# Kernel optimization log

Hardware: AMD Instinct MI355X
Metric: run time of the kernel (lower is better)

The kernel has to match this reference:

```python
import jax, jax.numpy as jnp
import numpy as np

B, C, T, V, Ks = 32, 64, 64, 325, 2

def setup_inputs() -> dict:
    key = jax.random.key(0)
    k1, k2, k3, k4 = jax.random.split(key, 4)
    x = jax.random.normal(k1, (B, C, T, V), dtype=jnp.float32)
    gso = jax.random.normal(k2, (V, V), dtype=jnp.float32)
    weight = jax.random.normal(k3, (Ks, C, C), dtype=jnp.float32) * (1.0 / np.sqrt(C))
    bias = jax.random.normal(k4, (C,), dtype=jnp.float32) * 0.05
    return {"x": x, "gso": gso, "weight": weight, "bias": bias}

def reference(x, gso, weight, bias):
    # Align: c_in == c_out -> identity
    xp = jnp.transpose(x, (0, 2, 3, 1))            # [B, T, V, C]
    x1 = jnp.einsum('hi,btij->bthj', gso, xp)      # Chebyshev T1 = L @ x
    xs = jnp.stack([xp, x1], axis=2)               # [B, T, Ks, V, C]
    gc = jnp.einsum('btkhi,kij->bthj', xs, weight) + bias  # [B, T, V, C]
    out = jnp.transpose(gc, (0, 3, 1, 2)) + x      # residual, [B, C, T, V]
    return out
```

## Files before the change

### kernel.cpp

```cpp
#include <hip/hip_runtime.h>


typedef __bf16 bf16x8 __attribute__((ext_vector_type(8)));
typedef float f32x4 __attribute__((ext_vector_type(4)));

#define XROW 360
#define QROW 136
#define NFRAG 512

__device__ __forceinline__ float bf2f(unsigned short u) {
  union { unsigned int i; float f; } t;
  t.i = ((unsigned int)u) << 16;
  return t.f;
}
__device__ __forceinline__ unsigned short f2bf_hw(float f) {
  __bf16 b = (__bf16)f;
  union { __bf16 b; unsigned short u; } t;
  t.b = b;
  return t.u;
}

__global__ void prep_kernel(const float* __restrict__ gso,
                            const float* __restrict__ weight,
                            unsigned short* __restrict__ gfrag,
                            unsigned short* __restrict__ wt) {
  int idx = blockIdx.x * 256 + threadIdx.x;
  if (idx < 22 * 11 * NFRAG) {
    int fid = idx >> 9, r = idx & 511;
    int l = r >> 3, j = r & 7;
    int mt = fid / 11, s = fid - 11 * mt;
    int v = (mt << 4) + (l & 15);
    int u = (s << 5) + ((l >> 4) << 3) + j;
    unsigned short val = 0;
    if (v < 325 && u < 325) val = f2bf_hw(gso[v * 325 + u]);
    gfrag[idx] = val;
  }
  if (idx < 2 * 64 * 64) {
    int k = idx >> 12, r = idx & 4095, c = r >> 6, i = r & 63;
    wt[idx] = f2bf_hw(weight[(k << 12) | (i << 6) | c]);
  }
}

__global__ __launch_bounds__(1024, 4) void gconv_kernel(
    const float* __restrict__ x,
    const float* __restrict__ bias,
    const unsigned short* __restrict__ gfrag,
    const unsigned short* __restrict__ wt,
    float* __restrict__ out) {
  __shared__ unsigned short Xr[64 * XROW];
  __shared__ unsigned short XY[352 * QROW];

  const int bid = blockIdx.x;
  const int b = bid >> 6, t = bid & 63;
  const int tid = threadIdx.x;
  const int xbase = b * 1331200 + t * 325;

  {
    const int c1 = tid >> 4;
    const int u0 = tid & 15;
    const float* xrow = &x[xbase + c1 * 20800];
    unsigned short* xr = &Xr[c1 * XROW];
    unsigned short* xyc = &XY[c1];
#pragma unroll 11
    for (int k = 0; k < 22; ++k) {
      const int u = u0 + 16 * k;
      float val = (u < 325) ? xrow[u] : 0.f;
      unsigned short us = f2bf_hw(val);
      xr[u] = us;
      xyc[u * QROW] = us;
    }
  }
  __syncthreads();

  const int wid = tid >> 6, lane = tid & 63;
  const int quad = lane >> 4, l16 = lane & 15;
  const int koff = quad * 8;

  {
    const int cn = (wid & 1) * 32;
    bf16x8 bX0[11], bX1[11];
#pragma unroll
    for (int s = 0; s < 11; ++s) {
      bX0[s] = *reinterpret_cast<const bf16x8*>(&Xr[(cn + l16) * XROW + s * 32 + koff]);
      bX1[s] = *reinterpret_cast<const bf16x8*>(&Xr[(cn + 16 + l16) * XROW + s * 32 + koff]);
    }
    for (int mt = (wid >> 1); mt < 22; mt += 8) {
      const unsigned short* gp = &gfrag[(mt * 11) * NFRAG + lane * 8];
      f32x4 acc0 = {0.f, 0.f, 0.f, 0.f};
      f32x4 acc1 = {0.f, 0.f, 0.f, 0.f};
#pragma unroll
      for (int s = 0; s < 11; ++s) {
        bf16x8 ag = *reinterpret_cast<const bf16x8*>(gp + s * NFRAG);
        acc0 = __builtin_amdgcn_mfma_f32_16x16x32_bf16(ag, bX0[s], acc0, 0, 0, 0);
        acc1 = __builtin_amdgcn_mfma_f32_16x16x32_bf16(ag, bX1[s], acc1, 0, 0, 0);
      }
      const int vr = mt * 16 + quad * 4;
#pragma unroll
      for (int r = 0; r < 4; ++r) {
        XY[(vr + r) * QROW + 64 + cn + l16] = f2bf_hw(acc0[r]);
        XY[(vr + r) * QROW + 64 + cn + 16 + l16] = f2bf_hw(acc1[r]);
      }
    }
  }
  __syncthreads();

  {
    const int cb = (wid & 3) * 16;
    bf16x8 aW[4];
#pragma unroll
    for (int s = 0; s < 4; ++s)
      aW[s] = *reinterpret_cast<const bf16x8*>(
          &wt[((s >> 1) * 64 + cb + l16) * 64 + (s & 1) * 32 + koff]);
    float bias_f[4];
#pragma unroll
    for (int r = 0; r < 4; ++r) bias_f[r] = bias[cb + quad * 4 + r];

    for (int n = (wid >> 2); n < 22; n += 4) {
      const int vb = n * 16;
      const unsigned short* xyp = &XY[(vb + l16) * QROW];
      bf16x8 bx0 = *reinterpret_cast<const bf16x8*>(xyp + koff);
      bf16x8 bx1 = *reinterpret_cast<const bf16x8*>(xyp + 32 + koff);
      bf16x8 by0 = *reinterpret_cast<const bf16x8*>(xyp + 64 + koff);
      bf16x8 by1 = *reinterpret_cast<const bf16x8*>(xyp + 96 + koff);
      f32x4 acc = {0.f, 0.f, 0.f, 0.f};
      acc = __builtin_amdgcn_mfma_f32_16x16x32_bf16(aW[0], bx0, acc, 0, 0, 0);
      acc = __builtin_amdgcn_mfma_f32_16x16x32_bf16(aW[1], bx1, acc, 0, 0, 0);
      acc = __builtin_amdgcn_mfma_f32_16x16x32_bf16(aW[2], by0, acc, 0, 0, 0);
      acc = __builtin_amdgcn_mfma_f32_16x16x32_bf16(aW[3], by1, acc, 0, 0, 0);
      const int v = vb + l16;
      if (v < 325) {
        ushort4 rx = *reinterpret_cast<const ushort4*>(xyp + cb + quad * 4);
        const unsigned short rr[4] = {rx.x, rx.y, rx.z, rx.w};
#pragma unroll
        for (int r = 0; r < 4; ++r) {
          const int c = cb + quad * 4 + r;
          out[xbase + c * 20800 + v] = acc[r] + bias_f[r] + bf2f(rr[r]);
        }
      }
    }
  }
}

extern "C" void kernel_launch(void* const* d_in, const int* in_sizes, int n_in,
                              void* d_out, int out_size, void* d_ws, size_t ws_size,
                              hipStream_t stream) {
  const float* x      = (const float*)d_in[0];
  const float* gso    = (const float*)d_in[1];
  const float* weight = (const float*)d_in[2];
  const float* bias   = (const float*)d_in[3];
  unsigned short* gfrag = (unsigned short*)d_ws;
  unsigned short* wt    = gfrag + 22 * 11 * NFRAG;

  prep_kernel<<<485, 256, 0, stream>>>(gso, weight, gfrag, wt);
  gconv_kernel<<<2048, 1024, 0, stream>>>(x, bias, gfrag, wt, (float*)d_out);
}
```

Baseline: 385.1 us.

## Process eight time steps per block with register prefetch of next x slice

Each block now loops over 8 consecutive time steps instead of handling one, so the grid shrinks from 2048 to 256 blocks. Weights and bias are loaded once per block, and the next time step's x row is prefetched into registers while the output GEMM of the current step runs. The graph GEMM is restructured so each wave owns one or two row tiles across all 64 channels, sharing B fragments from LDS and reducing the tile count from 22 to 21. The cost is fewer blocks (256 on a chip with many CUs, one 1024-thread block each), which may limit latency hiding, plus an extra barrier per iteration.

```diff
diff --git a/kernel.cpp b/kernel.cpp
--- a/kernel.cpp
+++ b/kernel.cpp
@@ -7,6 +7,7 @@
 #define XROW 360
 #define QROW 136
 #define NFRAG 512
+#define NMT 21
 
 __device__ __forceinline__ float bf2f(unsigned short u) {
   union { unsigned int i; float f; } t;
@@ -51,71 +52,105 @@
   __shared__ unsigned short XY[352 * QROW];
 
   const int bid = blockIdx.x;
-  const int b = bid >> 6, t = bid & 63;
+  const int b = bid >> 3, tq = bid & 7;
   const int tid = threadIdx.x;
-  const int xbase = b * 1331200 + t * 325;
-
-  {
-    const int c1 = tid >> 4;
-    const int u0 = tid & 15;
-    const float* xrow = &x[xbase + c1 * 20800];
-    unsigned short* xr = &Xr[c1 * XROW];
-    unsigned short* xyc = &XY[c1];
-#pragma unroll 11
-    for (int k = 0; k < 22; ++k) {
-      const int u = u0 + 16 * k;
-      float val = (u < 325) ? xrow[u] : 0.f;
-      unsigned short us = f2bf_hw(val);
-      xr[u] = us;
-      xyc[u * QROW] = us;
-    }
-  }
-  __syncthreads();
-
   const int wid = tid >> 6, lane = tid & 63;
   const int quad = lane >> 4, l16 = lane & 15;
   const int koff = quad * 8;
 
-  {
-    const int cn = (wid & 1) * 32;
-    bf16x8 bX0[11], bX1[11];
+  const int c1 = tid >> 4, u0 = tid & 15;
+  const float* xrow0 = &x[(size_t)b * 1331200 + c1 * 20800 + (tq * 8) * 325];
+
+  const int cb = (wid & 3) * 16;
+  bf16x8 aW[4];
 #pragma unroll
-    for (int s = 0; s < 11; ++s) {
-      bX0[s] = *reinterpret_cast<const bf16x8*>(&Xr[(cn + l16) * XROW + s * 32 + koff]);
-      bX1[s] = *reinterpret_cast<const bf16x8*>(&Xr[(cn + 16 + l16) * XROW + s * 32 + koff]);
+  for (int s = 0; s < 4; ++s)
+    aW[s] = *reinterpret_cast<const bf16x8*>(
+        &wt[((s >> 1) * 64 + cb + l16) * 64 + (s & 1) * 32 + koff]);
+  float bias_f[4];
+#pragma unroll
+  for (int r = 0; r < 4; ++r) bias_f[r] = bias[cb + quad * 4 + r];
+
+  float xs[21];
+#pragma unroll
+  for (int k = 0; k < 20; ++k) xs[k] = xrow0[u0 + 16 * k];
+  xs[20] = (u0 < 5) ? xrow0[u0 + 320] : 0.f;
+
+  for (int it = 0; it < 8; ++it) {
+    const int t = tq * 8 + it;
+    const int xbase = b * 1331200 + t * 325;
+
+    {
+      unsigned short* xrp = &Xr[c1 * XROW];
+      unsigned short* xyc = &XY[c1];
+#pragma unroll
+      for (int k = 0; k < 21; ++k) {
+        const int u = u0 + 16 * k;
+        unsigned short us = f2bf_hw(xs[k]);
+        xrp[u] = us;
+        xyc[u * QROW] = us;
+      }
+      const int u = u0 + 336;
+      xrp[u] = 0;
+      xyc[u * QROW] = 0;
     }
-    for (int mt = (wid >> 1); mt < 22; mt += 8) {
-      const unsigned short* gp = &gfrag[(mt * 11) * NFRAG + lane * 8];
-      f32x4 acc0 = {0.f, 0.f, 0.f, 0.f};
-      f32x4 acc1 = {0.f, 0.f, 0.f, 0.f};
+    __syncthreads();
+
+    {
+      const int mt0 = wid, mt1 = wid + 16;
+      const bool two = (mt1 < NMT);
+      const unsigned short* gp0 = &gfrag[(mt0 * 11) * NFRAG + lane * 8];
+      const unsigned short* gp1 = &gfrag[(mt1 * 11) * NFRAG + lane * 8];
+      f32x4 acc0[4], acc1[4];
+#pragma unroll
+      for (int q = 0; q < 4; ++q) {
+        acc0[q] = (f32x4){0.f, 0.f, 0.f, 0.f};
+        acc1[q] = (f32x4){0.f, 0.f, 0.f, 0.f};
+      }
 #pragma unroll
       for (int s = 0; s < 11; ++s) {
-        bf16x8 ag = *reinterpret_cast<const bf16x8*>(gp + s * NFRAG);
-        acc0 = __builtin_amdgcn_mfma_f32_16x16x32_bf16(ag, bX0[s], acc0, 0, 0, 0);
-        acc1 = __builtin_amdgcn_mfma_f32_16x16x32_bf16(ag, bX1[s], acc1, 0, 0, 0);
+        bf16x8 bXq[4];
+#pragma unroll
+        for (int q = 0; q < 4; ++q)
+          bXq[q] = *reinterpret_cast<const bf16x8*>(
+              &Xr[(q * 16 + l16) * XROW + s * 32 + koff]);
+        bf16x8 ag0 = *reinterpret_cast<const bf16x8*>(gp0 + s * NFRAG);
+#pragma unroll
+        for (int q = 0; q < 4; ++q)
+          acc0[q] = __builtin_amdgcn_mfma_f32_16x16x32_bf16(ag0, bXq[q], acc0[q], 0, 0, 0);
+        if (two) {
+          bf16x8 ag1 = *reinterpret_cast<const bf16x8*>(gp1 + s * NFRAG);
+#pragma unroll
+          for (int q = 0; q < 4; ++q)
+            acc1[q] = __builtin_amdgcn_mfma_f32_16x16x32_bf16(ag1, bXq[q], acc1[q], 0, 0, 0);
+        }
       }
-      const int vr = mt * 16 + quad * 4;
+      const int vr0 = mt0 * 16 + quad * 4;
 #pragma unroll
-      for (int r = 0; r < 4; ++r) {
-        XY[(vr + r) * QROW + 64 + cn + l16] = f2bf_hw(acc0[r]);
-        XY[(vr + r) * QROW + 64 + cn + 16 + l16] = f2bf_hw(acc1[r]);
+      for (int q = 0; q < 4; ++q)
+#pragma unroll
+        for (int r = 0; r < 4; ++r)
+          XY[(vr0 + r) * QROW + 64 + q * 16 + l16] = f2bf_hw(acc0[q][r]);
+      if (two) {
+        const int vr1 = mt1 * 16 + quad * 4;
+#pragma unroll
+        for (int q = 0; q < 4; ++q)
+#pragma unroll
+          for (int r = 0; r < 4; ++r)
+            XY[(vr1 + r) * QROW + 64 + q * 16 + l16] = f2bf_hw(acc1[q][r]);
       }
     }
-  }
-  __syncthreads();
+    __syncthreads();
 
-  {
-    const int cb = (wid & 3) * 16;
-    bf16x8 aW[4];
+    if (it < 7) {
+      const float* xr = xrow0 + (it + 1) * 325;
 #pragma unroll
-    for (int s = 0; s < 4; ++s)
-      aW[s] = *reinterpret_cast<const bf16x8*>(
-          &wt[((s >> 1) * 64 + cb + l16) * 64 + (s & 1) * 32 + koff]);
-    float bias_f[4];
-#pragma unroll
-    for (int r = 0; r < 4; ++r) bias_f[r] = bias[cb + quad * 4 + r];
+      for (int k = 0; k < 20; ++k) xs[k] = xr[u0 + 16 * k];
+      xs[20] = (u0 < 5) ? xr[u0 + 320] : 0.f;
+      __builtin_amdgcn_sched_barrier(0);
+    }
 
-    for (int n = (wid >> 2); n < 22; n += 4) {
+    for (int n = (wid >> 2); n < NMT; n += 4) {
       const int vb = n * 16;
       const unsigned short* xyp = &XY[(vb + l16) * QROW];
       bf16x8 bx0 = *reinterpret_cast<const bf16x8*>(xyp + koff);
@@ -138,6 +173,7 @@
         }
       }
     }
+    __syncthreads();
   }
 }
 
@@ -152,5 +188,5 @@
   unsigned short* wt    = gfrag + 22 * 11 * NFRAG;
 
   prep_kernel<<<485, 256, 0, stream>>>(gso, weight, gfrag, wt);
-  gconv_kernel<<<2048, 1024, 0, stream>>>(x, bias, gfrag, wt, (float*)d_out);
+  gconv_kernel<<<256, 1024, 0, stream>>>(x, bias, gfrag, wt, (float*)d_out);
 }
```

Result: slower. 489.2 us (+27.0%).

## Split each (b,t) slice across two blocks by vertex half and shrink LDS

Applied to the files above, without the earlier changes.

Each block now computes only half of the output vertices for a (b,t) slice, doubling the grid. The transposed X buffer shrinks to the block's half, and the graph-product result reuses the Xr buffer after its fragments are loaded into registers. The goal is lower LDS per block and higher occupancy (launch bounds raised to 8). The cost is that every block still loads and converts the full x slice, so global reads and the conversion work are duplicated.

```diff
diff --git a/kernel.cpp b/kernel.cpp
--- a/kernel.cpp
+++ b/kernel.cpp
@@ -5,7 +5,7 @@
 typedef float f32x4 __attribute__((ext_vector_type(4)));
 
 #define XROW 360
-#define QROW 136
+#define TROW 72
 #define NFRAG 512
 
 __device__ __forceinline__ float bf2f(unsigned short u) {
@@ -41,17 +41,22 @@
   }
 }
 
-__global__ __launch_bounds__(1024, 4) void gconv_kernel(
+__global__ __launch_bounds__(1024, 8) void gconv_kernel(
     const float* __restrict__ x,
     const float* __restrict__ bias,
     const unsigned short* __restrict__ gfrag,
     const unsigned short* __restrict__ wt,
     float* __restrict__ out) {
   __shared__ unsigned short Xr[64 * XROW];
-  __shared__ unsigned short XY[352 * QROW];
+  __shared__ unsigned short Xt[176 * TROW];
+  unsigned short* const Yt = Xr;
 
   const int bid = blockIdx.x;
-  const int b = bid >> 6, t = bid & 63;
+  const int h = bid & 1;
+  const int bt = bid >> 1;
+  const int b = bt >> 6, t = bt & 63;
+  const int nmt = 11 - h;
+  const int voff = h * 176;
   const int tid = threadIdx.x;
   const int xbase = b * 1331200 + t * 325;
 
@@ -59,15 +64,15 @@
     const int c1 = tid >> 4;
     const int u0 = tid & 15;
     const float* xrow = &x[xbase + c1 * 20800];
-    unsigned short* xr = &Xr[c1 * XROW];
-    unsigned short* xyc = &XY[c1];
-#pragma unroll 11
+    unsigned short* xrp = &Xr[c1 * XROW];
+#pragma unroll
     for (int k = 0; k < 22; ++k) {
       const int u = u0 + 16 * k;
       float val = (u < 325) ? xrow[u] : 0.f;
       unsigned short us = f2bf_hw(val);
-      xr[u] = us;
-      xyc[u * QROW] = us;
+      xrp[u] = us;
+      const int vl = u - voff;
+      if (vl >= 0 && vl < 176) Xt[vl * TROW + c1] = us;
     }
   }
   __syncthreads();
@@ -76,31 +81,26 @@
   const int quad = lane >> 4, l16 = lane & 15;
   const int koff = quad * 8;
 
-  {
-    const int cn = (wid & 1) * 32;
-    bf16x8 bX0[11], bX1[11];
+  const int cn = (wid & 3) * 16;
+  bf16x8 bX[11];
+#pragma unroll
+  for (int s = 0; s < 11; ++s)
+    bX[s] = *reinterpret_cast<const bf16x8*>(&Xr[(cn + l16) * XROW + s * 32 + koff]);
+  __syncthreads();
+
+  for (int lt = (wid >> 2); lt < nmt; lt += 4) {
+    const int mt = h * 11 + lt;
+    const unsigned short* gp = &gfrag[(mt * 11) * NFRAG + lane * 8];
+    f32x4 acc = {0.f, 0.f, 0.f, 0.f};
 #pragma unroll
     for (int s = 0; s < 11; ++s) {
-      bX0[s] = *reinterpret_cast<const bf16x8*>(&Xr[(cn + l16) * XROW + s * 32 + koff]);
-      bX1[s] = *reinterpret_cast<const bf16x8*>(&Xr[(cn + 16 + l16) * XROW + s * 32 + koff]);
+      bf16x8 ag = *reinterpret_cast<const bf16x8*>(gp + s * NFRAG);
+      acc = __builtin_amdgcn_mfma_f32_16x16x32_bf16(ag, bX[s], acc, 0, 0, 0);
     }
-    for (int mt = (wid >> 1); mt < 22; mt += 8) {
-      const unsigned short* gp = &gfrag[(mt * 11) * NFRAG + lane * 8];
-      f32x4 acc0 = {0.f, 0.f, 0.f, 0.f};
-      f32x4 acc1 = {0.f, 0.f, 0.f, 0.f};
+    const int vlr = lt * 16 + quad * 4;
 #pragma unroll
-      for (int s = 0; s < 11; ++s) {
-        bf16x8 ag = *reinterpret_cast<const bf16x8*>(gp + s * NFRAG);
-        acc0 = __builtin_amdgcn_mfma_f32_16x16x32_bf16(ag, bX0[s], acc0, 0, 0, 0);
-        acc1 = __builtin_amdgcn_mfma_f32_16x16x32_bf16(ag, bX1[s], acc1, 0, 0, 0);
-      }
-      const int vr = mt * 16 + quad * 4;
-#pragma unroll
-      for (int r = 0; r < 4; ++r) {
-        XY[(vr + r) * QROW + 64 + cn + l16] = f2bf_hw(acc0[r]);
-        XY[(vr + r) * QROW + 64 + cn + 16 + l16] = f2bf_hw(acc1[r]);
-      }
-    }
+    for (int r = 0; r < 4; ++r)
+      Yt[(vlr + r) * TROW + cn + l16] = f2bf_hw(acc[r]);
   }
   __syncthreads();
 
@@ -115,21 +115,23 @@
 #pragma unroll
     for (int r = 0; r < 4; ++r) bias_f[r] = bias[cb + quad * 4 + r];
 
-    for (int n = (wid >> 2); n < 22; n += 4) {
-      const int vb = n * 16;
-      const unsigned short* xyp = &XY[(vb + l16) * QROW];
-      bf16x8 bx0 = *reinterpret_cast<const bf16x8*>(xyp + koff);
-      bf16x8 bx1 = *reinterpret_cast<const bf16x8*>(xyp + 32 + koff);
-      bf16x8 by0 = *reinterpret_cast<const bf16x8*>(xyp + 64 + koff);
-      bf16x8 by1 = *reinterpret_cast<const bf16x8*>(xyp + 96 + koff);
+    for (int nloc = (wid >> 2); nloc < nmt; nloc += 4) {
+      const int vbl = nloc * 16;
+      const unsigned short* tp = &Xt[(vbl + l16) * TROW + koff];
+      const unsigned short* yp = &Yt[(vbl + l16) * TROW + koff];
+      bf16x8 bx0 = *reinterpret_cast<const bf16x8*>(tp);
+      bf16x8 bx1 = *reinterpret_cast<const bf16x8*>(tp + 32);
+      bf16x8 by0 = *reinterpret_cast<const bf16x8*>(yp);
+      bf16x8 by1 = *reinterpret_cast<const bf16x8*>(yp + 32);
       f32x4 acc = {0.f, 0.f, 0.f, 0.f};
       acc = __builtin_amdgcn_mfma_f32_16x16x32_bf16(aW[0], bx0, acc, 0, 0, 0);
       acc = __builtin_amdgcn_mfma_f32_16x16x32_bf16(aW[1], bx1, acc, 0, 0, 0);
       acc = __builtin_amdgcn_mfma_f32_16x16x32_bf16(aW[2], by0, acc, 0, 0, 0);
       acc = __builtin_amdgcn_mfma_f32_16x16x32_bf16(aW[3], by1, acc, 0, 0, 0);
-      const int v = vb + l16;
+      const int v = voff + vbl + l16;
       if (v < 325) {
-        ushort4 rx = *reinterpret_cast<const ushort4*>(xyp + cb + quad * 4);
+        ushort4 rx = *reinterpret_cast<const ushort4*>(
+            &Xt[(vbl + l16) * TROW + cb + quad * 4]);
         const unsigned short rr[4] = {rx.x, rx.y, rx.z, rx.w};
 #pragma unroll
         for (int r = 0; r < 4; ++r) {
@@ -152,5 +154,5 @@
   unsigned short* wt    = gfrag + 22 * 11 * NFRAG;
 
   prep_kernel<<<485, 256, 0, stream>>>(gso, weight, gfrag, wt);
-  gconv_kernel<<<2048, 1024, 0, stream>>>(x, bias, gfrag, wt, (float*)d_out);
+  gconv_kernel<<<4096, 1024, 0, stream>>>(x, bias, gfrag, wt, (float*)d_out);
 }
```

New measurement: 467.4 us. 1.21x slower.

## Reassociate graph conv: apply Ks=1 weight before the graph multiply

Applied to the files above, without the earlier changes.

The kernel now computes Z = W1ᵀ·x over channels first and then multiplies Z by the graph operator, instead of computing L·x and then mixing channels. The k=0 weight product is fused into the accumulator that seeds the graph multiply, so the concatenated XY buffer is gone. x is staged into LDS once, in transposed layout, and the LDS footprint shrinks. The intent is fewer LDS writes and a smaller shared-memory footprint. In exchange, the bf16 rounding point moves to the intermediate Z, and the gfrag tile is reused as the B operand.

```diff
diff --git a/kernel.cpp b/kernel.cpp
--- a/kernel.cpp
+++ b/kernel.cpp
@@ -4,9 +4,10 @@
 typedef __bf16 bf16x8 __attribute__((ext_vector_type(8)));
 typedef float f32x4 __attribute__((ext_vector_type(4)));
 
-#define XROW 360
-#define QROW 136
+#define XTROW 68
+#define ZROW 360
 #define NFRAG 512
+#define NMT 21
 
 __device__ __forceinline__ float bf2f(unsigned short u) {
   union { unsigned int i; float f; } t;
@@ -47,8 +48,8 @@
     const unsigned short* __restrict__ gfrag,
     const unsigned short* __restrict__ wt,
     float* __restrict__ out) {
-  __shared__ unsigned short Xr[64 * XROW];
-  __shared__ unsigned short XY[352 * QROW];
+  __shared__ unsigned short Xt[336 * XTROW];
+  __shared__ unsigned short Z[64 * ZROW];
 
   const int bid = blockIdx.x;
   const int b = bid >> 6, t = bid & 63;
@@ -59,82 +60,82 @@
     const int c1 = tid >> 4;
     const int u0 = tid & 15;
     const float* xrow = &x[xbase + c1 * 20800];
-    unsigned short* xr = &Xr[c1 * XROW];
-    unsigned short* xyc = &XY[c1];
-#pragma unroll 11
-    for (int k = 0; k < 22; ++k) {
+#pragma unroll
+    for (int k = 0; k < 21; ++k) {
       const int u = u0 + 16 * k;
       float val = (u < 325) ? xrow[u] : 0.f;
-      unsigned short us = f2bf_hw(val);
-      xr[u] = us;
-      xyc[u * QROW] = us;
+      Xt[u * XTROW + c1] = f2bf_hw(val);
     }
   }
+  for (int i = tid; i < 64 * 24; i += 1024)
+    Z[(i / 24) * ZROW + 336 + (i % 24)] = 0;
   __syncthreads();
 
   const int wid = tid >> 6, lane = tid & 63;
   const int quad = lane >> 4, l16 = lane & 15;
   const int koff = quad * 8;
+  const int cb = (wid & 3) * 16;
+  const int w4 = wid >> 2;
 
-  {
-    const int cn = (wid & 1) * 32;
-    bf16x8 bX0[11], bX1[11];
+  bf16x8 aW0[2], aW1[2];
 #pragma unroll
-    for (int s = 0; s < 11; ++s) {
-      bX0[s] = *reinterpret_cast<const bf16x8*>(&Xr[(cn + l16) * XROW + s * 32 + koff]);
-      bX1[s] = *reinterpret_cast<const bf16x8*>(&Xr[(cn + 16 + l16) * XROW + s * 32 + koff]);
-    }
-    for (int mt = (wid >> 1); mt < 22; mt += 8) {
-      const unsigned short* gp = &gfrag[(mt * 11) * NFRAG + lane * 8];
-      f32x4 acc0 = {0.f, 0.f, 0.f, 0.f};
-      f32x4 acc1 = {0.f, 0.f, 0.f, 0.f};
+  for (int s = 0; s < 2; ++s) {
+    aW0[s] = *reinterpret_cast<const bf16x8*>(&wt[(cb + l16) * 64 + s * 32 + koff]);
+    aW1[s] = *reinterpret_cast<const bf16x8*>(&wt[(64 + cb + l16) * 64 + s * 32 + koff]);
+  }
+
+  f32x4 p0[6];
 #pragma unroll
-      for (int s = 0; s < 11; ++s) {
-        bf16x8 ag = *reinterpret_cast<const bf16x8*>(gp + s * NFRAG);
-        acc0 = __builtin_amdgcn_mfma_f32_16x16x32_bf16(ag, bX0[s], acc0, 0, 0, 0);
-        acc1 = __builtin_amdgcn_mfma_f32_16x16x32_bf16(ag, bX1[s], acc1, 0, 0, 0);
-      }
-      const int vr = mt * 16 + quad * 4;
+  for (int j = 0; j < 6; ++j) {
+    p0[j] = (f32x4){0.f, 0.f, 0.f, 0.f};
+    const int nt = w4 + 4 * j;
+    if (nt < NMT) {
+      const unsigned short* tp = &Xt[(nt * 16 + l16) * XTROW];
+      bf16x8 b0 = *reinterpret_cast<const bf16x8*>(tp + koff);
+      bf16x8 b1 = *reinterpret_cast<const bf16x8*>(tp + 32 + koff);
+      f32x4 z = {0.f, 0.f, 0.f, 0.f};
+      z = __builtin_amdgcn_mfma_f32_16x16x32_bf16(aW1[0], b0, z, 0, 0, 0);
+      z = __builtin_amdgcn_mfma_f32_16x16x32_bf16(aW1[1], b1, z, 0, 0, 0);
+      p0[j] = __builtin_amdgcn_mfma_f32_16x16x32_bf16(aW0[0], b0, p0[j], 0, 0, 0);
+      p0[j] = __builtin_amdgcn_mfma_f32_16x16x32_bf16(aW0[1], b1, p0[j], 0, 0, 0);
 #pragma unroll
-      for (int r = 0; r < 4; ++r) {
-        XY[(vr + r) * QROW + 64 + cn + l16] = f2bf_hw(acc0[r]);
-        XY[(vr + r) * QROW + 64 + cn + 16 + l16] = f2bf_hw(acc1[r]);
-      }
+      for (int r = 0; r < 4; ++r)
+        Z[(cb + quad * 4 + r) * ZROW + nt * 16 + l16] = f2bf_hw(z[r]);
     }
   }
   __syncthreads();
 
   {
-    const int cb = (wid & 3) * 16;
-    bf16x8 aW[4];
+    bf16x8 zA[11];
 #pragma unroll
-    for (int s = 0; s < 4; ++s)
-      aW[s] = *reinterpret_cast<const bf16x8*>(
-          &wt[((s >> 1) * 64 + cb + l16) * 64 + (s & 1) * 32 + koff]);
+    for (int s = 0; s < 11; ++s)
+      zA[s] = *reinterpret_cast<const bf16x8*>(&Z[(cb + l16) * ZROW + s * 32 + koff]);
     float bias_f[4];
 #pragma unroll
     for (int r = 0; r < 4; ++r) bias_f[r] = bias[cb + quad * 4 + r];
 
-    for (int n = (wid >> 2); n < 22; n += 4) {
-      const int vb = n * 16;
-      const unsigned short* xyp = &XY[(vb + l16) * QROW];
-      bf16x8 bx0 = *reinterpret_cast<const bf16x8*>(xyp + koff);
-      bf16x8 bx1 = *reinterpret_cast<const bf16x8*>(xyp + 32 + koff);
-      bf16x8 by0 = *reinterpret_cast<const bf16x8*>(xyp + 64 + koff);
-      bf16x8 by1 = *reinterpret_cast<const bf16x8*>(xyp + 96 + koff);
-      f32x4 acc = {0.f, 0.f, 0.f, 0.f};
-      acc = __builtin_amdgcn_mfma_f32_16x16x32_bf16(aW[0], bx0, acc, 0, 0, 0);
-      acc = __builtin_amdgcn_mfma_f32_16x16x32_bf16(aW[1], bx1, acc, 0, 0, 0);
-      acc = __builtin_amdgcn_mfma_f32_16x16x32_bf16(aW[2], by0, acc, 0, 0, 0);
-      acc = __builtin_amdgcn_mfma_f32_16x16x32_bf16(aW[3], by1, acc, 0, 0, 0);
-      const int v = vb + l16;
-      if (v < 325) {
-        ushort4 rx = *reinterpret_cast<const ushort4*>(xyp + cb + quad * 4);
-        const unsigned short rr[4] = {rx.x, rx.y, rx.z, rx.w};
 #pragma unroll
-        for (int r = 0; r < 4; ++r) {
-          const int c = cb + quad * 4 + r;
-          out[xbase + c * 20800 + v] = acc[r] + bias_f[r] + bf2f(rr[r]);
+    for (int j = 0; j < 6; ++j) {
+      const int nt = w4 + 4 * j;
+      if (nt < NMT) {
+        const int vb = nt * 16;
+        const unsigned short* gp = &gfrag[(nt * 11) * NFRAG + lane * 8];
+        f32x4 acc = p0[j];
+#pragma unroll
+        for (int s = 0; s < 11; ++s) {
+          bf16x8 bg = *reinterpret_cast<const bf16x8*>(gp + s * NFRAG);
+          acc = __builtin_amdgcn_mfma_f32_16x16x32_bf16(zA[s], bg, acc, 0, 0, 0);
+        }
+        const int v = vb + l16;
+        if (v < 325) {
+          ushort4 rx = *reinterpret_cast<const ushort4*>(
+              &Xt[(vb + l16) * XTROW + cb + quad * 4]);
+          const unsigned short rr[4] = {rx.x, rx.y, rx.z, rx.w};
+#pragma unroll
+          for (int r = 0; r < 4; ++r) {
+            const int c = cb + quad * 4 + r;
+            out[xbase + c * 20800 + v] = acc[r] + bias_f[r] + bf2f(rr[r]);
+          }
         }
       }
     }
```

Result: slower. 443.6 us (+15.2%).
